# Performance work log

Measured on AMD Instinct MI355X. Metric: run time of the kernel, lower is better.

The kernel has to match this reference:

```python
import jax, jax.numpy as jnp
import numpy as np

ANGSTROM_TO_BOHR = 1.8897261258369282
CUTOFF = 5.2  # angstrom
N_SPECIES = 4  # H, C, N, O

# GFN1-xTB-style per-element constants for (H, C, N, O)
_ALPHA = np.array([2.209700, 1.247655, 1.524329, 1.845886], dtype=np.float32)
_Y_EFF = np.array([1.116244, 4.428763, 5.498808, 5.171786], dtype=np.float32)


def _smooth_cutoff(d, rc, eps=1e-10):
    # torchani 'smooth' cutoff: exp(1 - 1/(1 - (d/rc)^2)) for d < rc, else 0
    x2 = (d / rc) ** 2
    e = 1.0 - 1.0 / jnp.maximum(1.0 - x2, eps)
    return jnp.where(d < rc, jnp.exp(e), jnp.zeros_like(d))


def setup_inputs() -> dict:
    key = jax.random.key(0)
    k1, k2, k3 = jax.random.split(key, 3)
    M, A, P = 2048, 64, 8388608
    element_idxs = jax.random.randint(k1, (M, A), 0, N_SPECIES, dtype=jnp.int64)
    neighbor_idxs = jax.random.randint(k2, (2, P), 0, M * A, dtype=jnp.int64)
    distances = jax.random.uniform(k3, (P,), dtype=jnp.float32, minval=0.5, maxval=6.0)
    # precomputed pairwise parameter tables (buffers in the torch module)
    y_ab = jnp.asarray(np.outer(_Y_EFF, _Y_EFF))                 # [4,4]
    sqrt_alpha_ab = jnp.asarray(np.sqrt(np.outer(_ALPHA, _ALPHA)))  # [4,4]
    k_rep = np.full((N_SPECIES, N_SPECIES), 1.5, dtype=np.float32)
    k_rep[0, 0] = 1.0  # H-H
    k_rep_ab = jnp.asarray(k_rep)
    return {
        "element_idxs": element_idxs,
        "neighbor_idxs": neighbor_idxs,
        "distances": distances,
        "y_ab": y_ab,
        "sqrt_alpha_ab": sqrt_alpha_ab,
        "k_rep_ab": k_rep_ab,
    }


def reference(element_idxs, neighbor_idxs, distances, y_ab, sqrt_alpha_ab, k_rep_ab):
    M, A = element_idxs.shape
    d = jnp.clip(distances, 1e-7) * ANGSTROM_TO_BOHR  # [P] bohr
    species12 = element_idxs.reshape(-1)[neighbor_idxs]  # [2, P]
    s0, s1 = species12[0], species12[1]
    y = y_ab[s0, s1]                    # [P] gather
    sa = sqrt_alpha_ab[s0, s1]          # [P]
    kr = k_rep_ab[s0, s1]               # [P]
    rep = (y / d) * jnp.exp(-sa * d ** kr)
    rep = rep * _smooth_cutoff(d, CUTOFF * ANGSTROM_TO_BOHR)
    mol_idx = neighbor_idxs[0] // A     # [P]
    energies = jax.ops.segment_sum(rep, mol_idx, num_segments=M)  # [M]
    return energies
```

## Files before the change

### kernel.cpp

```cpp
#include <hip/hip_runtime.h>


#define AB_D 1.8897261258369282
#define L2E  1.4426950408889634f

__global__ __launch_bounds__(256) void pack_zero_kernel(
    const int* __restrict__ elem, int natoms, int nwords,
    unsigned* __restrict__ packed, float* __restrict__ out, int M)
{
    int g = blockIdx.x * blockDim.x + threadIdx.x;
    if (g < M) out[g] = 0.0f;
    if (packed != nullptr && g < nwords) {
        int base = g * 16;
        unsigned w = 0u;
        if (base + 16 <= natoms) {
            const int4* p = (const int4*)(elem + base);
            #pragma unroll
            for (int q = 0; q < 4; ++q) {
                int4 v = p[q];
                w |= ((unsigned)v.x & 3u) << (2 * (4 * q + 0));
                w |= ((unsigned)v.y & 3u) << (2 * (4 * q + 1));
                w |= ((unsigned)v.z & 3u) << (2 * (4 * q + 2));
                w |= ((unsigned)v.w & 3u) << (2 * (4 * q + 3));
            }
        } else {
            for (int j = 0; j < 16; ++j) {
                int a = base + j;
                unsigned s = (a < natoms) ? ((unsigned)elem[a] & 3u) : 0u;
                w |= s << (2 * j);
            }
        }
        packed[g] = w;
    }
}

__global__ __launch_bounds__(1024, 8) void rep_main_kernel(
    const int* __restrict__ nbr, const float* __restrict__ dist,
    const unsigned* __restrict__ packed_g,
    const float* __restrict__ y_ab, const float* __restrict__ sa_ab,
    const float* __restrict__ kr_ab,
    long long P, int M, int nwords, int ashift, int A,
    float* __restrict__ partials, float* __restrict__ out,
    int mode )
{
    extern __shared__ char smem[];
    float*  acc = (float*)smem;
    float2* tbl = (float2*)(smem + (size_t)M * 4);
    unsigned* pk = (unsigned*)(smem + (size_t)M * 4 + 16 * sizeof(float2));

    const int tid = threadIdx.x;
    const int nthr = blockDim.x;

    for (int m = tid; m < M; m += nthr) acc[m] = 0.0f;
    for (int w = tid; w < nwords; w += nthr) pk[w] = packed_g[w];
    if (tid < 16) {
        float sa = sa_ab[tid] * L2E;
        if (kr_ab[tid] == 1.0f) sa = -sa;
        tbl[tid] = make_float2(y_ab[tid], sa);
    }
    __syncthreads();

    const float ABf   = (float)AB_D;
    const float DMIN  = (float)(1e-7 * AB_D);
    const float RCINV = (float)(1.0 / (5.2 * AB_D));

    const int4*   nb04 = (const int4*)nbr;
    const int4*   nb14 = (const int4*)(nbr + P);
    const float4* dv4  = (const float4*)dist;

    long long P8 = P >> 3;
    long long gstride = (long long)gridDim.x * nthr;
    for (long long g = (long long)blockIdx.x * nthr + tid; g < P8; g += gstride) {
        long long q = g << 1;
        int4   i0a = nb04[q];     int4   i0b = nb04[q + 1];
        int4   i1a = nb14[q];     int4   i1b = nb14[q + 1];
        float4 da  = dv4[q];      float4 db  = dv4[q + 1];

        unsigned a0[8] = {(unsigned)i0a.x,(unsigned)i0a.y,(unsigned)i0a.z,(unsigned)i0a.w,
                          (unsigned)i0b.x,(unsigned)i0b.y,(unsigned)i0b.z,(unsigned)i0b.w};
        unsigned a1[8] = {(unsigned)i1a.x,(unsigned)i1a.y,(unsigned)i1a.z,(unsigned)i1a.w,
                          (unsigned)i1b.x,(unsigned)i1b.y,(unsigned)i1b.z,(unsigned)i1b.w};
        float dr[8] = {da.x,da.y,da.z,da.w, db.x,db.y,db.z,db.w};

        unsigned w0[8], w1[8];
        #pragma unroll
        for (int j = 0; j < 8; ++j) {
            w0[j] = pk[a0[j] >> 4];
            w1[j] = pk[a1[j] >> 4];
        }

        float2   t[8];
        unsigned mol[8];
        #pragma unroll
        for (int j = 0; j < 8; ++j) {
            unsigned s0 = (w0[j] >> ((a0[j] & 15u) * 2u)) & 3u;
            unsigned s1 = (w1[j] >> ((a1[j] & 15u) * 2u)) & 3u;
            t[j] = tbl[s0 * 4u + s1];
            mol[j] = (ashift >= 0) ? (a0[j] >> ashift) : (a0[j] / (unsigned)A);
        }

        float rep[8];
        #pragma unroll
        for (int j = 0; j < 8; ++j) {
            float d   = fmaxf(dr[j] * ABf, DMIN);
            float x   = d * RCINV;
            float om  = fmaxf(fmaf(-x, x, 1.0f), 0.0f);
            float r   = __builtin_amdgcn_rcpf(om);
            float e   = fmaf(-L2E, r, L2E);
            float sq  = __builtin_amdgcn_sqrtf(d);
            float fac = (t[j].y < 0.0f) ? 1.0f : sq;
            float arg = fmaf(-fabsf(t[j].y), d * fac, e);
            float ex  = __builtin_amdgcn_exp2f(arg);
            rep[j] = t[j].x * __builtin_amdgcn_rcpf(d) * ex;
        }

        #pragma unroll
        for (int j = 0; j < 8; ++j)
            atomicAdd(&acc[mol[j]], rep[j]);
    }

    long long tail0 = P8 << 3;
    if (blockIdx.x == 0) {
        const int* nb0 = nbr;
        const int* nb1 = nbr + P;
        for (long long p = tail0 + tid; p < P; p += nthr) {
            unsigned ua0 = (unsigned)nb0[p], ua1 = (unsigned)nb1[p];
            float d = fmaxf(dist[p] * ABf, DMIN);
            unsigned s0 = (pk[ua0 >> 4] >> ((ua0 & 15u) * 2u)) & 3u;
            unsigned s1 = (pk[ua1 >> 4] >> ((ua1 & 15u) * 2u)) & 3u;
            float2 t = tbl[s0 * 4u + s1];
            float x   = d * RCINV;
            float om  = fmaxf(fmaf(-x, x, 1.0f), 0.0f);
            float r   = __builtin_amdgcn_rcpf(om);
            float e   = fmaf(-L2E, r, L2E);
            float sq  = __builtin_amdgcn_sqrtf(d);
            float fac = (t.y < 0.0f) ? 1.0f : sq;
            float arg = fmaf(-fabsf(t.y), d * fac, e);
            float ex  = __builtin_amdgcn_exp2f(arg);
            float rep = t.x * __builtin_amdgcn_rcpf(d) * ex;
            unsigned mol = (ashift >= 0) ? (ua0 >> ashift) : (ua0 / (unsigned)A);
            atomicAdd(&acc[mol], rep);
        }
    }
    __syncthreads();

    if (mode == 0) {
        float* row = partials + (size_t)blockIdx.x * (size_t)M;
        for (int m = tid; m < M; m += nthr) row[m] = acc[m];
    } else {
        for (int m = tid; m < M; m += nthr) {
            float v = acc[m];
            if (v != 0.0f) atomicAdd(&out[m], v);
        }
    }
}

__global__ __launch_bounds__(256) void reduce_kernel(
    const float* __restrict__ partials, float* __restrict__ out,
    int M, int nblk, int rows_per)
{
    int m = blockIdx.x * blockDim.x + threadIdx.x;
    if (m >= M) return;
    int r0 = blockIdx.y * rows_per;
    int r1 = r0 + rows_per;
    if (r1 > nblk) r1 = nblk;
    if (r0 >= r1) return;
    float s0 = 0.f, s1 = 0.f, s2 = 0.f, s3 = 0.f;
    int r = r0;
    for (; r + 3 < r1; r += 4) {
        s0 += partials[(size_t)(r + 0) * M + m];
        s1 += partials[(size_t)(r + 1) * M + m];
        s2 += partials[(size_t)(r + 2) * M + m];
        s3 += partials[(size_t)(r + 3) * M + m];
    }
    for (; r < r1; ++r) s0 += partials[(size_t)r * M + m];
    atomicAdd(&out[m], (s0 + s1) + (s2 + s3));
}

extern "C" void kernel_launch(void* const* d_in, const int* in_sizes, int n_in,
                              void* d_out, int out_size, void* d_ws, size_t ws_size,
                              hipStream_t stream)
{
    const int*   elem  = (const int*)d_in[0];
    const int*   nbr   = (const int*)d_in[1];
    const float* dist  = (const float*)d_in[2];
    const float* y_ab  = (const float*)d_in[3];
    const float* sa_ab = (const float*)d_in[4];
    const float* kr_ab = (const float*)d_in[5];
    float* out = (float*)d_out;

    const int natoms = in_sizes[0];
    const long long P = (long long)in_sizes[2];
    const int M = out_size;
    const int A = natoms / M;
    int ashift = -1;
    if (A > 0 && (A & (A - 1)) == 0) {
        int s = 0;
        while ((1 << s) < A) ++s;
        ashift = s;
    }
    const int nwords = (natoms + 15) / 16;

    size_t packed_bytes = ((size_t)nwords * 4 + 255) & ~(size_t)255;
    bool have_packed = (ws_size >= packed_bytes);
    unsigned* packed = have_packed ? (unsigned*)d_ws : nullptr;
    if (!have_packed) return;

    const int BLOCK = 1024;
    int nblk = 512;
    float* partials = nullptr;
    int mode = 1;
    {
        size_t avail = ws_size - packed_bytes;
        size_t rowb = (size_t)M * 4;
        long long maxrows = (long long)(avail / rowb);
        if (maxrows >= 64) {
            nblk = (int)(maxrows < 512 ? maxrows : 512);
            partials = (float*)((char*)d_ws + packed_bytes);
            mode = 0;
        }
    }

    {
        int total = (nwords > M) ? nwords : M;
        int g = (total + 255) / 256;
        hipLaunchKernelGGL(pack_zero_kernel, dim3(g), dim3(256), 0, stream,
                           elem, natoms, nwords, packed, out, M);
    }

    {
        size_t smem = (size_t)M * 4 + 16 * sizeof(float2) + (size_t)nwords * 4;
        hipLaunchKernelGGL(rep_main_kernel, dim3(nblk), dim3(BLOCK), smem, stream,
                           nbr, dist, packed, y_ab, sa_ab, kr_ab,
                           P, M, nwords, ashift, A, partials, out, mode);
    }

    if (mode == 0) {
        const int SPLIT = 32;
        int rows_per = (nblk + SPLIT - 1) / SPLIT;
        dim3 grid((M + 255) / 256, SPLIT);
        hipLaunchKernelGGL(reduce_kernel, grid, dim3(256), 0, stream,
                           partials, out, M, nblk, rows_per);
    }
}
```

Before: 159.0 us.

## Coalesce loads across grid-stride pairs, add sched barriers, magic-multiply molecule index

Each thread previously read two adjacent int4/float4 vectors. Now it processes two vectors that are one grid stride apart, so every wave's loads stay fully contiguous, and a remainder loop handles the leftover quads. Scheduling barriers pin the order as LDS gathers first, then table lookups, then math. The power-of-two shift or integer divide for the molecule index becomes a 64-bit magic multiply and shift by 42, which adds a 64-bit multiply per pair and assumes indices are small enough for the magic to be exact.

```diff
diff --git a/kernel.cpp b/kernel.cpp
--- a/kernel.cpp
+++ b/kernel.cpp
@@ -39,7 +39,7 @@
     const unsigned* __restrict__ packed_g,
     const float* __restrict__ y_ab, const float* __restrict__ sa_ab,
     const float* __restrict__ kr_ab,
-    long long P, int M, int nwords, int ashift, int A,
+    long long P, int M, int nwords, unsigned long long molMagic, int A,
     float* __restrict__ partials, float* __restrict__ out,
     int mode )
 {
@@ -68,13 +68,15 @@
     const int4*   nb14 = (const int4*)(nbr + P);
     const float4* dv4  = (const float4*)dist;
 
-    long long P8 = P >> 3;
+    long long P4 = P >> 2;
     long long gstride = (long long)gridDim.x * nthr;
-    for (long long g = (long long)blockIdx.x * nthr + tid; g < P8; g += gstride) {
-        long long q = g << 1;
-        int4   i0a = nb04[q];     int4   i0b = nb04[q + 1];
-        int4   i1a = nb14[q];     int4   i1b = nb14[q + 1];
-        float4 da  = dv4[q];      float4 db  = dv4[q + 1];
+    long long i = (long long)blockIdx.x * nthr + tid;
+
+    for (; i + gstride < P4; i += 2 * gstride) {
+        long long qa = i, qb = i + gstride;
+        int4   i0a = nb04[qa];    int4   i0b = nb04[qb];
+        int4   i1a = nb14[qa];    int4   i1b = nb14[qb];
+        float4 da  = dv4[qa];     float4 db  = dv4[qb];
 
         unsigned a0[8] = {(unsigned)i0a.x,(unsigned)i0a.y,(unsigned)i0a.z,(unsigned)i0a.w,
                           (unsigned)i0b.x,(unsigned)i0b.y,(unsigned)i0b.z,(unsigned)i0b.w};
@@ -88,6 +90,7 @@
             w0[j] = pk[a0[j] >> 4];
             w1[j] = pk[a1[j] >> 4];
         }
+        __builtin_amdgcn_sched_barrier(0);
 
         float2   t[8];
         unsigned mol[8];
@@ -96,8 +99,9 @@
             unsigned s0 = (w0[j] >> ((a0[j] & 15u) * 2u)) & 3u;
             unsigned s1 = (w1[j] >> ((a1[j] & 15u) * 2u)) & 3u;
             t[j] = tbl[s0 * 4u + s1];
-            mol[j] = (ashift >= 0) ? (a0[j] >> ashift) : (a0[j] / (unsigned)A);
-        }
+            mol[j] = (unsigned)(((unsigned long long)a0[j] * molMagic) >> 42);
+        }
+        __builtin_amdgcn_sched_barrier(0);
 
         float rep[8];
         #pragma unroll
@@ -119,7 +123,34 @@
             atomicAdd(&acc[mol[j]], rep[j]);
     }
 
-    long long tail0 = P8 << 3;
+    for (; i < P4; i += gstride) {
+        int4   i0 = nb04[i];
+        int4   i1 = nb14[i];
+        float4 dv = dv4[i];
+        unsigned a0[4] = {(unsigned)i0.x,(unsigned)i0.y,(unsigned)i0.z,(unsigned)i0.w};
+        unsigned a1[4] = {(unsigned)i1.x,(unsigned)i1.y,(unsigned)i1.z,(unsigned)i1.w};
+        float dr[4] = {dv.x,dv.y,dv.z,dv.w};
+        #pragma unroll
+        for (int j = 0; j < 4; ++j) {
+            unsigned s0 = (pk[a0[j] >> 4] >> ((a0[j] & 15u) * 2u)) & 3u;
+            unsigned s1 = (pk[a1[j] >> 4] >> ((a1[j] & 15u) * 2u)) & 3u;
+            float2 t = tbl[s0 * 4u + s1];
+            float d   = fmaxf(dr[j] * ABf, DMIN);
+            float x   = d * RCINV;
+            float om  = fmaxf(fmaf(-x, x, 1.0f), 0.0f);
+            float r   = __builtin_amdgcn_rcpf(om);
+            float e   = fmaf(-L2E, r, L2E);
+            float sq  = __builtin_amdgcn_sqrtf(d);
+            float fac = (t.y < 0.0f) ? 1.0f : sq;
+            float arg = fmaf(-fabsf(t.y), d * fac, e);
+            float ex  = __builtin_amdgcn_exp2f(arg);
+            float rep = t.x * __builtin_amdgcn_rcpf(d) * ex;
+            unsigned mol = (unsigned)(((unsigned long long)a0[j] * molMagic) >> 42);
+            atomicAdd(&acc[mol], rep);
+        }
+    }
+
+    long long tail0 = P4 << 2;
     if (blockIdx.x == 0) {
         const int* nb0 = nbr;
         const int* nb1 = nbr + P;
@@ -138,7 +169,7 @@
             float arg = fmaf(-fabsf(t.y), d * fac, e);
             float ex  = __builtin_amdgcn_exp2f(arg);
             float rep = t.x * __builtin_amdgcn_rcpf(d) * ex;
-            unsigned mol = (ashift >= 0) ? (ua0 >> ashift) : (ua0 / (unsigned)A);
+            unsigned mol = (unsigned)(((unsigned long long)ua0 * molMagic) >> 42);
             atomicAdd(&acc[mol], rep);
         }
     }
@@ -193,12 +224,10 @@
     const long long P = (long long)in_sizes[2];
     const int M = out_size;
     const int A = natoms / M;
-    int ashift = -1;
-    if (A > 0 && (A & (A - 1)) == 0) {
-        int s = 0;
-        while ((1 << s) < A) ++s;
-        ashift = s;
-    }
+    unsigned long long molMagic =
+        (A > 0) ? ((((unsigned long long)1 << 42) + (unsigned long long)A - 1)
+                   / (unsigned long long)A)
+                : 1ull;
     const int nwords = (natoms + 15) / 16;
 
     size_t packed_bytes = ((size_t)nwords * 4 + 255) & ~(size_t)255;
@@ -232,7 +261,7 @@
         size_t smem = (size_t)M * 4 + 16 * sizeof(float2) + (size_t)nwords * 4;
         hipLaunchKernelGGL(rep_main_kernel, dim3(nblk), dim3(BLOCK), smem, stream,
                            nbr, dist, packed, y_ab, sa_ab, kr_ab,
-                           P, M, nwords, ashift, A, partials, out, mode);
+                           P, M, nwords, molMagic, A, partials, out, mode);
     }
 
     if (mode == 0) {
```

Result: no change. 158.4 us (-0.4%).
